# Optimization experiments

Measured on AMD Instinct MI355X. Metric: run time of the kernel, lower is better.

Reference implementation:

```python
import jax, jax.numpy as jnp
import numpy as np

B, T, U, F, H, V = 4, 512, 96, 512, 512, 256
NEG_INF = -1e30


def setup_inputs() -> dict:
    key = jax.random.key(0)
    ks = jax.random.split(key, 7)
    frames = jax.random.normal(ks[0], (B, T, F), dtype=jnp.float32)
    # guarantee num_frames >= num_labels so a valid alignment path exists
    num_frames = jax.random.randint(ks[1], (B,), T // 2, T + 1, dtype=jnp.int32)
    labels = jax.random.randint(ks[2], (B, U), 1, V + 1, dtype=jnp.int32)
    num_labels = jax.random.randint(ks[3], (B,), U // 2, U + 1, dtype=jnp.int32)
    scale = 0.02
    Wf = scale * jax.random.normal(ks[4], (F, H), dtype=jnp.float32)
    E = scale * jax.random.normal(ks[5], (V + 1, H), dtype=jnp.float32)
    Wo = scale * jax.random.normal(ks[6], (H, V + 1), dtype=jnp.float32)
    return dict(frames=frames, num_frames=num_frames, labels=labels,
                num_labels=num_labels, Wf=Wf, E=E, Wo=Wo)


def _lattice_loss(frames, num_frames, labels, num_labels, Wf, E, Wo):
    Bd, Td, _ = frames.shape
    Ud = labels.shape[1]
    # 1-gram context dependency: context state after u emitted labels is
    # 0 (start) if u == 0 else labels[u-1].  ctx: [B, U+1]
    ctx = jnp.concatenate([jnp.zeros((Bd, 1), labels.dtype), labels], axis=1)
    # locally normalized weight fn (RNN-T style joint network)
    fproj = jnp.einsum('btf,fh->bth', frames, Wf)                 # [B,T,H]
    cemb = jnp.take(E, ctx, axis=0)                               # [B,U+1,H]
    h = jnp.tanh(fproj[:, :, None, :] + cemb[:, None, :, :])      # [B,T,U+1,H]
    logits = jax.nn.log_softmax(
        jnp.einsum('btuh,hv->btuv', h, Wo), axis=-1)              # [B,T,U+1,V+1]
    blank = logits[..., 0]                                        # [B,T,U+1]
    # lexical arc weight for emitting label u+1 from state u:
    # lex[b,t,u] = logits[b,t,u, labels[b,u]]
    idx = jnp.broadcast_to(labels[:, None, :, None].astype(jnp.int32),
                           (Bd, Td, Ud, 1))
    lex = jnp.take_along_axis(logits[:, :, :Ud, :], idx, axis=3)[..., 0]  # [B,T,U]

    # forward DP under the Log semiring over the (t, u) string lattice
    alpha0 = jnp.full((Bd, Ud + 1), NEG_INF, dtype=logits.dtype).at[:, 0].set(0.0)

    def step(alpha, xs):
        blank_t, lex_t, t = xs  # [B,U+1], [B,U], scalar
        stay = alpha + blank_t
        emit = jnp.concatenate(
            [jnp.full((Bd, 1), NEG_INF, dtype=alpha.dtype),
             alpha[:, :-1] + lex_t], axis=1)
        new = jnp.logaddexp(stay, emit)
        new = jnp.where((t < num_frames)[:, None], new, alpha)
        return new, None

    xs = (jnp.swapaxes(blank, 0, 1), jnp.swapaxes(lex, 0, 1), jnp.arange(Td))
    alpha, _ = jax.lax.scan(step, alpha0, xs)
    logp = jnp.take_along_axis(alpha, num_labels[:, None].astype(jnp.int32),
                               axis=1)[:, 0]
    return -logp  # [B] negative sequence log-probability


def reference(frames, num_frames, labels, num_labels, Wf, E, Wo):
    return _lattice_loss(frames, num_frames, labels, num_labels, Wf, E, Wo)
```

## Files before the change

kernel.cpp:

```cpp
#include <hip/hip_runtime.h>
#include <hip/hip_bf16.h>


#define BB 4
#define TT 512
#define UU 96
#define FF 512
#define HH 512
#define VV 256
#define NV (VV + 1)
#define NU (UU + 1)
#define NP 288
#define NEG_INF (-1e30f)
#define LOG2E 1.4426950408889634f
#define LN2 0.6931471805599453f
#define NG 128
#define GSTRIDE 520
#define WOSCL 64.0f
#define INVWOSCL 0.015625f

typedef _Float16 f16;
typedef __attribute__((ext_vector_type(8))) _Float16 f16x8;
typedef __bf16 bf16;
typedef __bf16 bf16x8 __attribute__((ext_vector_type(8)));
typedef float f32x4 __attribute__((ext_vector_type(4)));

__device__ __forceinline__ f16x8 splat8(float s) {
    f16 v = (f16)s;
    f16x8 r = {v, v, v, v, v, v, v, v};
    return r;
}

__device__ __forceinline__ long tanh_pack8(f16x8 fv8, f16x8 cv8) {
    f16x8 x = fv8 + cv8;
    x = __builtin_elementwise_min(__builtin_elementwise_max(x, splat8(-2.0f)),
                                  splat8(2.0f));
    f16x8 y = x * x;
    f16x8 q = y * splat8(-0.0067528f) + splat8(0.0700672f);
    q = y * q + splat8(-0.301720f);
    q = y * q + splat8(1.0f);
    f16x8 t = x * q;
    int lo = 0, hi = 0;
    lo = __builtin_amdgcn_cvt_pk_fp8_f32((float)t[0], (float)t[1], lo, false);
    lo = __builtin_amdgcn_cvt_pk_fp8_f32((float)t[2], (float)t[3], lo, true);
    hi = __builtin_amdgcn_cvt_pk_fp8_f32((float)t[4], (float)t[5], hi, false);
    hi = __builtin_amdgcn_cvt_pk_fp8_f32((float)t[6], (float)t[7], hi, true);
    return (long)(((unsigned long long)(unsigned int)lo) |
                  (((unsigned long long)(unsigned int)hi) << 32));
}

__device__ __forceinline__ long pack_fp8x8(const float* v) {
    int lo = 0, hi = 0;
    lo = __builtin_amdgcn_cvt_pk_fp8_f32(v[0], v[1], lo, false);
    lo = __builtin_amdgcn_cvt_pk_fp8_f32(v[2], v[3], lo, true);
    hi = __builtin_amdgcn_cvt_pk_fp8_f32(v[4], v[5], hi, false);
    hi = __builtin_amdgcn_cvt_pk_fp8_f32(v[6], v[7], hi, true);
    return (long)(((unsigned long long)(unsigned int)lo) |
                  (((unsigned long long)(unsigned int)hi) << 32));
}

__device__ __forceinline__ float lae2(float x, float y) {
    float m = fmaxf(x, y);
    float d = fminf(x, y) - m;
    return m + __builtin_amdgcn_logf(1.0f + __builtin_amdgcn_exp2f(d));
}

__device__ __forceinline__ float lse3_2(float x, float y, float z) {
    float m = fmaxf(fmaxf(x, y), z);
    float s = __builtin_amdgcn_exp2f(x - m) + __builtin_amdgcn_exp2f(y - m) +
              __builtin_amdgcn_exp2f(z - m);
    return m + __builtin_amdgcn_logf(s);
}

__device__ __forceinline__ float lse5_2(float a, float b, float c, float d, float e) {
    float m = fmaxf(fmaxf(fmaxf(a, b), fmaxf(c, d)), e);
    float s = __builtin_amdgcn_exp2f(a - m) + __builtin_amdgcn_exp2f(b - m) +
              __builtin_amdgcn_exp2f(c - m) + __builtin_amdgcn_exp2f(d - m) +
              __builtin_amdgcn_exp2f(e - m);
    return m + __builtin_amdgcn_logf(s);
}

__device__ __forceinline__ void async_copy16(const void* g, void* l) {
    __builtin_amdgcn_global_load_lds(
        (const __attribute__((address_space(1))) unsigned int*)g,
        (__attribute__((address_space(3))) unsigned int*)l, 16, 0, 0);
}

__global__ __launch_bounds__(256, 2) void k_front(
    const float* __restrict__ frames, const float* __restrict__ Wf,
    const float* __restrict__ Wo, const float* __restrict__ E,
    const int* __restrict__ labels, f16* __restrict__ fproj,
    long* __restrict__ Wo_s, f16* __restrict__ cemb) {
    __shared__ bf16 Alds[64 * 40];
    __shared__ bf16 Blds[64 * 40];
    const int blk = blockIdx.x;
    const int tid = threadIdx.x;

    if (blk < 256) {
        const int r0 = (blk & 31) * 64;
        const int n0 = (blk >> 5) * 64;
        const int lane = tid & 63, w = tid >> 6;
        const int c = lane & 15, g = lane >> 4;

        const int srow = tid >> 2, sko = (tid & 3) * 8;
        const float* fptr = frames + (size_t)(r0 + srow) * FF + sko;
        const int q = tid >> 6, c64 = tid & 63;

        f32x4 acc[4];
#pragma unroll
        for (int j = 0; j < 4; ++j) acc[j] = (f32x4){0.f, 0.f, 0.f, 0.f};

        for (int kt = 0; kt < FF; kt += 32) {
            float4 f1 = *(const float4*)(fptr + kt);
            float4 f2 = *(const float4*)(fptr + kt + 4);
            bf16x8 av = {(bf16)f1.x, (bf16)f1.y, (bf16)f1.z, (bf16)f1.w,
                         (bf16)f2.x, (bf16)f2.y, (bf16)f2.z, (bf16)f2.w};
            *(bf16x8*)&Alds[srow * 40 + sko] = av;
#pragma unroll
            for (int p = 0; p < 8; ++p) {
                float v = Wf[(size_t)(kt + q * 8 + p) * HH + n0 + c64];
                Blds[c64 * 40 + q * 8 + p] = (bf16)v;
            }
            __syncthreads();
            const int m = w * 16;
            bf16x8 af = *(const bf16x8*)&Alds[(m + c) * 40 + g * 8];
#pragma unroll
            for (int j = 0; j < 4; ++j) {
                bf16x8 bv = *(const bf16x8*)&Blds[(j * 16 + c) * 40 + g * 8];
                acc[j] = __builtin_amdgcn_mfma_f32_16x16x32_bf16(af, bv, acc[j], 0, 0, 0);
            }
            __syncthreads();
        }
        const int m = w * 16;
#pragma unroll
        for (int j = 0; j < 4; ++j)
#pragma unroll
            for (int r = 0; r < 4; ++r)
                fproj[(size_t)(r0 + m + g * 4 + r) * HH + n0 + j * 16 + c] = (f16)acc[j][r];
    } else if (blk < 328) {
        int idx = (blk - 256) * 256 + tid;
        int n = idx % NP;
        int rest = idx / NP;
        int kg = rest & 3;
        int k32 = rest >> 2;
        float v[8];
#pragma unroll
        for (int e = 0; e < 8; ++e) {
            int k = k32 * 32 + kg * 8 + e;
            v[e] = (n < NV) ? Wo[k * NV + n] * WOSCL : 0.f;
        }
        Wo_s[idx] = pack_fp8x8(v);
    } else {
        int u = blk - 328;
        for (int b = 0; b < BB; ++b) {
            int ctx = (u == 0) ? 0 : labels[b * UU + (u - 1)];
            const float* src = E + (size_t)ctx * HH;
            f16* dst = cemb + ((size_t)b * NU + u) * HH;
            for (int i = tid; i < HH; i += 256) dst[i] = (f16)src[i];
        }
    }
}

__global__ __launch_bounds__(512, 4) void k_joint(
    const f16* __restrict__ fproj, const f16* __restrict__ cemb,
    const long* __restrict__ Wo_s, const int* __restrict__ labels,
    const int* __restrict__ num_frames, float* __restrict__ cl_arr) {
    __shared__ long A_s8[2][8 * 130];
    __shared__ long B_s8[2][2304];
    __shared__ float red[6 * 128];

    const int tid = threadIdx.x;
    const int b = blockIdx.y;
    const int r0 = blockIdx.x * 128;
    const int nf = num_frames[b];
    if (r0 / NU >= nf) return;

    const int lane = tid & 63, w = tid >> 6;
    const int wm = w & 3, wn = w >> 2;
    const int c = lane & 15, g = lane >> 4;

    const int arow = tid >> 2, akg = tid & 3;
    const int gr = r0 + arow;
    const int at = gr / NU, au = gr - at * NU;
    const f16* pf = fproj + ((size_t)(b * TT + at)) * HH + akg * 8;
    const f16* pc = cemb + ((size_t)(b * NU + au)) * HH + akg * 8;
    const int sdst8 = akg * 130 + arow;
    const char* wsrcB = (const char*)Wo_s + lane * 16;

    f32x4 acc[2][9];
#pragma unroll
    for (int mt = 0; mt < 2; ++mt)
#pragma unroll
        for (int j = 0; j < 9; ++j) acc[mt][j] = (f32x4){0.f, 0.f, 0.f, 0.f};

    const int aB0 = g * 130 + wm * 32 + c;
    const int bB0 = g * 288 + wn * 144 + c;

    {
        for (int ch = w; ch < 18; ch += 8)
            async_copy16(wsrcB + ch * 1024, (char*)&B_s8[0][0] + ch * 1024 + lane * 16);
        f16x8 fv0 = *(const f16x8*)pf;
        f16x8 cv0 = *(const f16x8*)pc;
        f16x8 fv1 = *(const f16x8*)(pf + 32);
        f16x8 cv1 = *(const f16x8*)(pc + 32);
        A_s8[0][sdst8] = tanh_pack8(fv0, cv0);
        A_s8[0][sdst8 + 520] = tanh_pack8(fv1, cv1);
        __syncthreads();
    }

    for (int i = 0; i < 8; ++i) {
        const int cur = i & 1, nxt = cur ^ 1;
        if (i < 7) {
            const char* wk = wsrcB + (size_t)(i + 1) * 18432;
            for (int ch = w; ch < 18; ch += 8)
                async_copy16(wk + ch * 1024, (char*)&B_s8[nxt][0] + ch * 1024 + lane * 16);
        }
#pragma unroll
        for (int s = 0; s < 2; ++s) {
            long af0 = A_s8[cur][aB0 + s * 520];
            long af1 = A_s8[cur][aB0 + s * 520 + 16];
#pragma unroll
            for (int j = 0; j < 9; ++j) {
                long bv = B_s8[cur][bB0 + s * 1152 + j * 16];
                acc[0][j] = __builtin_amdgcn_mfma_f32_16x16x32_fp8_fp8(af0, bv, acc[0][j], 0, 0, 0);
                acc[1][j] = __builtin_amdgcn_mfma_f32_16x16x32_fp8_fp8(af1, bv, acc[1][j], 0, 0, 0);
            }
        }
        if (i < 7) {
            const int kt = (i + 1) * 64;
            f16x8 fv0 = *(const f16x8*)(pf + kt);
            f16x8 cv0 = *(const f16x8*)(pc + kt);
            f16x8 fv1 = *(const f16x8*)(pf + kt + 32);
            f16x8 cv1 = *(const f16x8*)(pc + kt + 32);
            A_s8[nxt][sdst8] = tanh_pack8(fv0, cv0);
            A_s8[nxt][sdst8 + 520] = tanh_pack8(fv1, cv1);
        }
        __syncthreads();
    }

#pragma unroll
    for (int mt = 0; mt < 2; ++mt)
#pragma unroll
        for (int j = 0; j < 9; ++j) acc[mt][j] = acc[mt][j] * INVWOSCL;

    float* pmax0 = red;
    float* pmax1 = red + 128;
    float* psum0 = red + 256;
    float* psum1 = red + 384;
    float* pblank = red + 512;
    float* plex = red + 640;

#pragma unroll
    for (int mt = 0; mt < 2; ++mt) {
#pragma unroll
        for (int r = 0; r < 4; ++r) {
            int row_in = wm * 32 + mt * 16 + g * 4 + r;
            int grr = r0 + row_in;
            int u = grr - (grr / NU) * NU;

            float mx = NEG_INF;
#pragma unroll
            for (int j = 0; j < 9; ++j) {
                int col = wn * 144 + j * 16 + c;
                if (col < NV) mx = fmaxf(mx, acc[mt][j][r]);
            }
#pragma unroll
            for (int s = 1; s < 16; s <<= 1) mx = fmaxf(mx, __shfl_xor(mx, s));
            float sum = 0.f;
#pragma unroll
            for (int j = 0; j < 9; ++j) {
                int col = wn * 144 + j * 16 + c;
                if (col < NV) sum += __expf(acc[mt][j][r] - mx);
            }
#pragma unroll
            for (int s = 1; s < 16; s <<= 1) sum += __shfl_xor(sum, s);

            int L = (u < UU) ? labels[b * UU + u] : -1;
            int lc = L - wn * 144;
            bool own = (lc >= 0) && (lc < 144);
            int src = (lane & 48) | (lc & 15);
            int jl = lc >> 4;
            float lexv = 0.f;
#pragma unroll
            for (int j = 0; j < 9; ++j) {
                float cand = __shfl(acc[mt][j][r], src);
                if (j == jl) lexv = cand;
            }
            float blankv = __shfl(acc[mt][0][r], lane & 48);

            if (c == 0) {
                if (wn == 0) {
                    pmax0[row_in] = mx;
                    psum0[row_in] = sum;
                    pblank[row_in] = blankv;
                } else {
                    pmax1[row_in] = mx;
                    psum1[row_in] = sum;
                }
                if (own) plex[row_in] = lexv;
            }
        }
    }
    __syncthreads();
    if (tid < 128) {
        int grr = r0 + tid;
        int t = grr / NU, u = grr - t * NU;
        float m0 = pmax0[tid], m1 = pmax1[tid];
        float mx = fmaxf(m0, m1);
        float s = psum0[tid] * __expf(m0 - mx) + psum1[tid] * __expf(m1 - mx);
        float lse = mx + __logf(s);
        float2 v;
        v.x = pblank[tid] - lse;
        v.y = (u < UU) ? (plex[tid] - lse) : 0.f;
        *(float2*)&cl_arr[(((size_t)b * TT + t) * NU + u) * 2] = v;
    }
}

__global__ __launch_bounds__(128) void k_compact(
    const float* __restrict__ cl, const int* __restrict__ num_frames,
    float* __restrict__ Dg) {
    const int g = blockIdx.x;
    const int b = blockIdx.y;
    const int u = threadIdx.x;
    if (u >= NU) return;
    const int nf = num_frames[b];
    const float2* P = (const float2*)(cl + (size_t)b * TT * NU * 2);

    auto fetch = [&](int t, int uu, float& bb, float& ll) {
        if (uu <= UU) {
            float2 z = P[t * NU + uu];
            bool act = t < nf;
            bb = act ? z.x * LOG2E : 0.f;
            ll = (act && uu < UU) ? z.y * LOG2E : NEG_INF;
        } else {
            bb = NEG_INF;
            ll = NEG_INF;
        }
    };

    const int t0 = g * 4;
    float b0, l0, b1u, l1u, b1u1, l1u1;
    fetch(t0, u, b0, l0);
    fetch(t0 + 1, u, b1u, l1u);
    fetch(t0 + 1, u + 1, b1u1, l1u1);
    float A0 = b0 + b1u;
    float A1 = lae2(l0 + b1u1, b0 + l1u);
    float A2 = l0 + l1u1;
    float B0[3], B1[3], B2[3];
#pragma unroll
    for (int j = 0; j < 3; ++j) {
        float b2v, l2v, b3v, l3v, b3n, l3n;
        fetch(t0 + 2, u + j, b2v, l2v);
        fetch(t0 + 3, u + j, b3v, l3v);
        fetch(t0 + 3, u + j + 1, b3n, l3n);
        B0[j] = b2v + b3v;
        B1[j] = lae2(l2v + b3n, b2v + l3v);
        B2[j] = l2v + l3n;
    }
    float* d = Dg + ((size_t)b * NG + g) * GSTRIDE;
    d[u] = A0 + B0[0];
    d[104 + u] = lae2(A1 + B0[1], A0 + B1[0]);
    d[208 + u] = lse3_2(A2 + B0[2], A1 + B1[1], A0 + B2[0]);
    d[312 + u] = lae2(A2 + B1[2], A1 + B2[1]);
    d[416 + u] = A2 + B2[2];
}

__global__ __launch_bounds__(64) void k_dpser(
    const float* __restrict__ Dg, const int* __restrict__ num_labels,
    float* __restrict__ out) {
    const int b = blockIdx.x;
    const int lane = threadIdx.x;
    const float* D = Dg + (size_t)b * NG * GSTRIDE;
    const int lo_u = lane;
    const int hi_u = 64 + ((lane < 33) ? lane : 0);

    float a_lo = (lane == 0) ? 0.f : NEG_INF;
    float a_hi = NEG_INF;

    constexpr int R = 8;
    float blo[R][5], bhi[R][5];
#pragma unroll
    for (int g = 0; g < R; ++g)
#pragma unroll
        for (int k = 0; k < 5; ++k) {
            blo[g][k] = D[g * GSTRIDE + k * 104 + lo_u];
            bhi[g][k] = D[g * GSTRIDE + k * 104 + hi_u];
        }

#pragma unroll 8
    for (int g = 0; g < NG; ++g) {
        const int slot = g & (R - 1);
        float el[5], eh[5];
#pragma unroll
        for (int k = 0; k < 5; ++k) {
            el[k] = a_lo + blo[slot][k];
            eh[k] = a_hi + bhi[slot][k];
        }
        const int gp = g + R;
        if (gp < NG) {
#pragma unroll
            for (int k = 0; k < 5; ++k) {
                blo[slot][k] = D[gp * GSTRIDE + k * 104 + lo_u];
                bhi[slot][k] = D[gp * GSTRIDE + k * 104 + hi_u];
            }
        }
        float ml[5], mh[5];
        ml[0] = el[0];
        mh[0] = eh[0];
#pragma unroll
        for (int k = 1; k < 5; ++k) {
            float su = __shfl_up(el[k], k);
            ml[k] = (lane >= k) ? su : NEG_INF;
            float sh = __shfl_up(eh[k], k);
            float xl = __shfl(el[k], 64 - k + lane);
            mh[k] = (lane >= k) ? sh : xl;
        }
        a_lo = lse5_2(ml[0], ml[1], ml[2], ml[3], ml[4]);
        float nh = lse5_2(mh[0], mh[1], mh[2], mh[3], mh[4]);
        if (lane < 33) a_hi = nh;
    }

    const int nl = num_labels[b];
    float res = (nl < 64) ? __shfl(a_lo, nl) : __shfl(a_hi, nl - 64);
    if (lane == 0) out[b] = -res * LN2;
}

extern "C" void kernel_launch(void* const* d_in, const int* in_sizes, int n_in,
                              void* d_out, int out_size, void* d_ws, size_t ws_size,
                              hipStream_t stream) {
    const float* frames = (const float*)d_in[0];
    const int* num_frames = (const int*)d_in[1];
    const int* labels = (const int*)d_in[2];
    const int* num_labels = (const int*)d_in[3];
    const float* Wf = (const float*)d_in[4];
    const float* E = (const float*)d_in[5];
    const float* Wo = (const float*)d_in[6];
    float* out = (float*)d_out;

    char* ws = (char*)d_ws;
    size_t off = 0;
    long* Wo_s = (long*)(ws + off); off += (size_t)18432 * 8;
    f16* cemb = (f16*)(ws + off); off += (size_t)BB * NU * HH * 2;
    off = (off + 255) & ~(size_t)255;
    f16* fproj = (f16*)(ws + off); off += (size_t)BB * TT * HH * 2;
    off = (off + 255) & ~(size_t)255;
    float* cl_arr = (float*)(ws + off); off += (size_t)BB * TT * NU * 2 * 4;
    off = (off + 255) & ~(size_t)255;
    float* Dg = (float*)(ws + off); off += (size_t)BB * NG * GSTRIDE * 4;

    hipLaunchKernelGGL(k_front, dim3(425), dim3(256), 0, stream,
                       frames, Wf, Wo, E, labels, fproj, Wo_s, cemb);
    hipLaunchKernelGGL(k_joint, dim3((TT * NU) / 128, BB), dim3(512), 0, stream,
                       fproj, cemb, Wo_s, labels, num_frames, cl_arr);
    hipLaunchKernelGGL(k_compact, dim3(NG, BB), dim3(128), 0, stream,
                       cl_arr, num_frames, Dg);
    hipLaunchKernelGGL(k_dpser, dim3(BB), dim3(64), 0, stream,
                       Dg, num_labels, out);
}
```

Baseline: 203.4 us.

## Give each wave full-width rows with register-resident A fragments in joint kernel

Changes the joint GEMM tiling so each wave owns 16 rows across all 288 output columns, instead of a 4x2 wave grid. Each lane now computes its tanh-packed fp8 A fragment directly in registers, which removes the A shared-memory buffer. The softmax max, sum and lex/blank extraction are done within the wave using shuffles, which removes the cross-wave LDS reduction and its extra barrier. The compute loops are also wrapped in s_setprio. The cost is that every wave reads the whole B tile from LDS, doubling B reads per wave.

```diff
diff --git a/kernel.cpp b/kernel.cpp
--- a/kernel.cpp
+++ b/kernel.cpp
@@ -165,9 +165,7 @@
     const f16* __restrict__ fproj, const f16* __restrict__ cemb,
     const long* __restrict__ Wo_s, const int* __restrict__ labels,
     const int* __restrict__ num_frames, float* __restrict__ cl_arr) {
-    __shared__ long A_s8[2][8 * 130];
     __shared__ long B_s8[2][2304];
-    __shared__ float red[6 * 128];
 
     const int tid = threadIdx.x;
     const int b = blockIdx.y;
@@ -176,25 +174,21 @@
     if (r0 / NU >= nf) return;
 
     const int lane = tid & 63, w = tid >> 6;
-    const int wm = w & 3, wn = w >> 2;
     const int c = lane & 15, g = lane >> 4;
 
-    const int arow = tid >> 2, akg = tid & 3;
-    const int gr = r0 + arow;
+    const int gr = r0 + w * 16 + c;
     const int at = gr / NU, au = gr - at * NU;
-    const f16* pf = fproj + ((size_t)(b * TT + at)) * HH + akg * 8;
-    const f16* pc = cemb + ((size_t)(b * NU + au)) * HH + akg * 8;
-    const int sdst8 = akg * 130 + arow;
+    const f16* pf = fproj + ((size_t)(b * TT + at)) * HH + g * 8;
+    const f16* pc = cemb + ((size_t)(b * NU + au)) * HH + g * 8;
     const char* wsrcB = (const char*)Wo_s + lane * 16;
 
-    f32x4 acc[2][9];
-#pragma unroll
-    for (int mt = 0; mt < 2; ++mt)
-#pragma unroll
-        for (int j = 0; j < 9; ++j) acc[mt][j] = (f32x4){0.f, 0.f, 0.f, 0.f};
-
-    const int aB0 = g * 130 + wm * 32 + c;
-    const int bB0 = g * 288 + wn * 144 + c;
+    f32x4 acc[18];
+#pragma unroll
+    for (int j = 0; j < 18; ++j) acc[j] = (f32x4){0.f, 0.f, 0.f, 0.f};
+
+    const int bB0 = g * 288 + c;
+
+    long a0, a1;
 
     {
         for (int ch = w; ch < 18; ch += 8)
@@ -203,116 +197,89 @@
         f16x8 cv0 = *(const f16x8*)pc;
         f16x8 fv1 = *(const f16x8*)(pf + 32);
         f16x8 cv1 = *(const f16x8*)(pc + 32);
-        A_s8[0][sdst8] = tanh_pack8(fv0, cv0);
-        A_s8[0][sdst8 + 520] = tanh_pack8(fv1, cv1);
+        a0 = tanh_pack8(fv0, cv0);
+        a1 = tanh_pack8(fv1, cv1);
         __syncthreads();
     }
 
     for (int i = 0; i < 8; ++i) {
         const int cur = i & 1, nxt = cur ^ 1;
+        f16x8 fv0, cv0, fv1, cv1;
         if (i < 7) {
             const char* wk = wsrcB + (size_t)(i + 1) * 18432;
             for (int ch = w; ch < 18; ch += 8)
                 async_copy16(wk + ch * 1024, (char*)&B_s8[nxt][0] + ch * 1024 + lane * 16);
         }
-#pragma unroll
-        for (int s = 0; s < 2; ++s) {
-            long af0 = A_s8[cur][aB0 + s * 520];
-            long af1 = A_s8[cur][aB0 + s * 520 + 16];
-#pragma unroll
-            for (int j = 0; j < 9; ++j) {
-                long bv = B_s8[cur][bB0 + s * 1152 + j * 16];
-                acc[0][j] = __builtin_amdgcn_mfma_f32_16x16x32_fp8_fp8(af0, bv, acc[0][j], 0, 0, 0);
-                acc[1][j] = __builtin_amdgcn_mfma_f32_16x16x32_fp8_fp8(af1, bv, acc[1][j], 0, 0, 0);
-            }
-        }
+        __builtin_amdgcn_s_setprio(1);
+#pragma unroll
+        for (int j = 0; j < 18; ++j) {
+            long bv = B_s8[cur][bB0 + j * 16];
+            acc[j] = __builtin_amdgcn_mfma_f32_16x16x32_fp8_fp8(a0, bv, acc[j], 0, 0, 0);
+        }
+        __builtin_amdgcn_s_setprio(0);
         if (i < 7) {
             const int kt = (i + 1) * 64;
-            f16x8 fv0 = *(const f16x8*)(pf + kt);
-            f16x8 cv0 = *(const f16x8*)(pc + kt);
-            f16x8 fv1 = *(const f16x8*)(pf + kt + 32);
-            f16x8 cv1 = *(const f16x8*)(pc + kt + 32);
-            A_s8[nxt][sdst8] = tanh_pack8(fv0, cv0);
-            A_s8[nxt][sdst8 + 520] = tanh_pack8(fv1, cv1);
-        }
-        __syncthreads();
-    }
-
-#pragma unroll
-    for (int mt = 0; mt < 2; ++mt)
-#pragma unroll
-        for (int j = 0; j < 9; ++j) acc[mt][j] = acc[mt][j] * INVWOSCL;
-
-    float* pmax0 = red;
-    float* pmax1 = red + 128;
-    float* psum0 = red + 256;
-    float* psum1 = red + 384;
-    float* pblank = red + 512;
-    float* plex = red + 640;
-
-#pragma unroll
-    for (int mt = 0; mt < 2; ++mt) {
-#pragma unroll
-        for (int r = 0; r < 4; ++r) {
-            int row_in = wm * 32 + mt * 16 + g * 4 + r;
-            int grr = r0 + row_in;
-            int u = grr - (grr / NU) * NU;
-
-            float mx = NEG_INF;
-#pragma unroll
-            for (int j = 0; j < 9; ++j) {
-                int col = wn * 144 + j * 16 + c;
-                if (col < NV) mx = fmaxf(mx, acc[mt][j][r]);
-            }
-#pragma unroll
-            for (int s = 1; s < 16; s <<= 1) mx = fmaxf(mx, __shfl_xor(mx, s));
-            float sum = 0.f;
-#pragma unroll
-            for (int j = 0; j < 9; ++j) {
-                int col = wn * 144 + j * 16 + c;
-                if (col < NV) sum += __expf(acc[mt][j][r] - mx);
-            }
-#pragma unroll
-            for (int s = 1; s < 16; s <<= 1) sum += __shfl_xor(sum, s);
-
-            int L = (u < UU) ? labels[b * UU + u] : -1;
-            int lc = L - wn * 144;
-            bool own = (lc >= 0) && (lc < 144);
-            int src = (lane & 48) | (lc & 15);
-            int jl = lc >> 4;
-            float lexv = 0.f;
-#pragma unroll
-            for (int j = 0; j < 9; ++j) {
-                float cand = __shfl(acc[mt][j][r], src);
-                if (j == jl) lexv = cand;
-            }
-            float blankv = __shfl(acc[mt][0][r], lane & 48);
-
-            if (c == 0) {
-                if (wn == 0) {
-                    pmax0[row_in] = mx;
-                    psum0[row_in] = sum;
-                    pblank[row_in] = blankv;
-                } else {
-                    pmax1[row_in] = mx;
-                    psum1[row_in] = sum;
-                }
-                if (own) plex[row_in] = lexv;
-            }
-        }
-    }
-    __syncthreads();
-    if (tid < 128) {
-        int grr = r0 + tid;
-        int t = grr / NU, u = grr - t * NU;
-        float m0 = pmax0[tid], m1 = pmax1[tid];
-        float mx = fmaxf(m0, m1);
-        float s = psum0[tid] * __expf(m0 - mx) + psum1[tid] * __expf(m1 - mx);
-        float lse = mx + __logf(s);
-        float2 v;
-        v.x = pblank[tid] - lse;
-        v.y = (u < UU) ? (plex[tid] - lse) : 0.f;
-        *(float2*)&cl_arr[(((size_t)b * TT + t) * NU + u) * 2] = v;
+            fv0 = *(const f16x8*)(pf + kt);
+            cv0 = *(const f16x8*)(pc + kt);
+            fv1 = *(const f16x8*)(pf + kt + 32);
+            cv1 = *(const f16x8*)(pc + kt + 32);
+        }
+        __builtin_amdgcn_s_setprio(1);
+#pragma unroll
+        for (int j = 0; j < 18; ++j) {
+            long bv = B_s8[cur][bB0 + 1152 + j * 16];
+            acc[j] = __builtin_amdgcn_mfma_f32_16x16x32_fp8_fp8(a1, bv, acc[j], 0, 0, 0);
+        }
+        __builtin_amdgcn_s_setprio(0);
+        if (i < 7) {
+            a0 = tanh_pack8(fv0, cv0);
+            a1 = tanh_pack8(fv1, cv1);
+            __syncthreads();
+        }
+    }
+
+#pragma unroll
+    for (int j = 0; j < 18; ++j) acc[j] = acc[j] * INVWOSCL;
+
+    const int rbase = r0 + w * 16 + g * 4;
+#pragma unroll
+    for (int r = 0; r < 4; ++r) {
+        const int grr = rbase + r;
+        const int t = grr / NU, u = grr - t * NU;
+
+        float mx = NEG_INF;
+#pragma unroll
+        for (int j = 0; j < 17; ++j) {
+            int col = j * 16 + c;
+            if (col < NV) mx = fmaxf(mx, acc[j][r]);
+        }
+#pragma unroll
+        for (int s = 1; s < 16; s <<= 1) mx = fmaxf(mx, __shfl_xor(mx, s));
+        float sum = 0.f;
+#pragma unroll
+        for (int j = 0; j < 17; ++j) {
+            int col = j * 16 + c;
+            if (col < NV) sum += __expf(acc[j][r] - mx);
+        }
+#pragma unroll
+        for (int s = 1; s < 16; s <<= 1) sum += __shfl_xor(sum, s);
+        float lse = mx + __logf(sum);
+
+        float blankv = __shfl(acc[0][r], lane & 48);
+        int L = (u < UU) ? labels[b * UU + u] : 0;
+        int jl = L >> 4;
+        float v = acc[0][r];
+#pragma unroll
+        for (int j = 1; j < 17; ++j)
+            if (jl == j) v = acc[j][r];
+        float lexv = __shfl(v, (lane & 48) | (L & 15));
+
+        if (c == 0) {
+            float2 ov;
+            ov.x = blankv - lse;
+            ov.y = (u < UU) ? (lexv - lse) : 0.f;
+            *(float2*)&cl_arr[(((size_t)b * TT + t) * NU + u) * 2] = ov;
+        }
     }
 }
 
```

Measured after the change: 191.3 us. 1.06x faster.
